# Kernel optimization log

Hardware: AMD Instinct MI355X
Metric: run time of the kernel (lower is better)

## Reference

```python
import jax, jax.numpy as jnp
import numpy as np

SEQ_LEN, BATCH, INPUT_SIZE, HIDDEN = 512, 64, 256, 1024


def setup_inputs() -> dict:
    key = jax.random.key(0)
    ks = jax.random.split(key, 17)
    inp = {"x": jax.random.normal(ks[0], (SEQ_LEN, BATCH, INPUT_SIZE), dtype=jnp.float32)}
    # 8 Linear layers: odd-numbered take x (in=INPUT_SIZE), even-numbered take h (in=HIDDEN).
    sx = 1.0 / np.sqrt(INPUT_SIZE)
    sh = 1.0 / np.sqrt(HIDDEN)
    for i in range(1, 9):
        fan_in, scale = (INPUT_SIZE, sx) if i % 2 == 1 else (HIDDEN, sh)
        inp[f"W{i}"] = jax.random.uniform(ks[2 * i - 1], (fan_in, HIDDEN), jnp.float32, -scale, scale)
        inp[f"b{i}"] = jax.random.uniform(ks[2 * i], (HIDDEN,), jnp.float32, -scale, scale)
    return inp


def reference(x, W1, b1, W2, b2, W3, b3, W4, b4, W5, b5, W6, b6, W7, b7, W8, b8):
    # Gate order matching the torch module: out1(f-like)=lin1/lin2, out2(i)=lin3/lin4,
    # out3(o)=lin5/lin6, cand=lin7/lin8.  Fuse the 4 input-side GEMMs into one big GEMM
    # over all timesteps, and the 4 hidden-side GEMMs into one per-step GEMM.
    Wx = jnp.concatenate([W1, W3, W5, W7], axis=1)            # (I, 4H)
    bx = jnp.concatenate([b1, b3, b5, b7], axis=0)            # (4H,)
    Wh = jnp.concatenate([W2, W4, W6, W8], axis=1)            # (H, 4H)
    bh = jnp.concatenate([b2, b4, b6, b8], axis=0)            # (4H,)

    H = W2.shape[0]
    xg = jnp.einsum('sbi,ig->sbg', x, Wx) + bx + bh           # (S, B, 4H)

    def step(carry, xg_t):
        h, c = carry                                          # (B, H) each
        g = xg_t + h @ Wh                                     # (B, 4H)
        f = jax.nn.sigmoid(g[:, 0 * H:1 * H])
        i = jax.nn.sigmoid(g[:, 1 * H:2 * H])
        o = jax.nn.sigmoid(g[:, 2 * H:3 * H])
        cand = jnp.tanh(g[:, 3 * H:4 * H])
        c = f * c + i * cand
        h = o * jnp.tanh(c)
        return (h, c), h

    B = x.shape[1]
    h0 = jnp.zeros((B, H), dtype=x.dtype)
    c0 = jnp.zeros((B, H), dtype=x.dtype)
    (h, c), h_seq = jax.lax.scan(step, (h0, c0), xg)
    # Torch module returns (h_seq, (h, c)) with h,c leading dim 1.
    return h_seq, (h[None], c[None])
```

## Files before the change

### kernel.cpp

```cpp
#include <hip/hip_runtime.h>


#define OFF_XB    0ul
#define OFF_WXP   16777216ul
#define OFF_WHP   18874368ul
#define OFF_BIAS  27262976ul
#define OFF_HBUF  27279360ul
#define OFF_FLG   27541504ul

typedef __attribute__((ext_vector_type(8))) __bf16 bf16x8;
typedef __attribute__((ext_vector_type(4))) float  floatx4;

struct KPtrs { const float* p[17]; };

__device__ __forceinline__ unsigned short f2bf(float f) {
  unsigned int u = __float_as_uint(f);
  u += 0x7fffu + ((u >> 16) & 1u);
  return (unsigned short)(u >> 16);
}

__device__ __forceinline__ bf16x8 ld16(const unsigned short* p) {
  return *(const bf16x8*)p;
}

__device__ __forceinline__ bf16x8 ldsys16(const unsigned short* p) {
  unsigned long long a =
      __hip_atomic_load((const unsigned long long*)p,       __ATOMIC_RELAXED, __HIP_MEMORY_SCOPE_AGENT);
  unsigned long long b =
      __hip_atomic_load((const unsigned long long*)(p + 4), __ATOMIC_RELAXED, __HIP_MEMORY_SCOPE_AGENT);
  unsigned long long arr[2] = {a, b};
  bf16x8 r;
  __builtin_memcpy(&r, arr, 16);
  return r;
}

__device__ __forceinline__ float fsig(float x) {
  return __builtin_amdgcn_rcpf(1.f + __expf(-x));
}
__device__ __forceinline__ float ftanh(float x) {
  return 1.f - 2.f * __builtin_amdgcn_rcpf(1.f + __expf(2.f * x));
}

__global__ void pack_kernel(KPtrs P, unsigned char* ws) {
  unsigned short* xb   = (unsigned short*)(ws + OFF_XB);
  unsigned short* wxp  = (unsigned short*)(ws + OFF_WXP);
  unsigned short* whp  = (unsigned short*)(ws + OFF_WHP);
  float*          bias = (float*)(ws + OFF_BIAS);
  unsigned int*   hb32 = (unsigned int*)(ws + OFF_HBUF);
  int*            flg  = (int*)(ws + OFF_FLG);
  const float* x = P.p[0];

  const long tid = (long)blockIdx.x * blockDim.x + threadIdx.x;
  const long nth = (long)gridDim.x * blockDim.x;

  for (long e = tid; e < 8388608l; e += nth)
    xb[e] = f2bf(x[e]);
  for (long e = tid; e < 1048576l; e += nth) {
    int c = (int)(e >> 8), i = (int)(e & 255);
    int gg = c >> 10, j = c & 1023;
    wxp[e] = f2bf(P.p[1 + 4 * gg][i * 1024 + j]);
  }
  for (long e = tid; e < 4194304l; e += nth) {
    int c = (int)(e >> 10), k = (int)(e & 1023);
    int gg = c >> 10, j = c & 1023;
    whp[e] = f2bf(P.p[3 + 4 * gg][k * 1024 + j]);
  }
  for (long e = tid; e < 4096l; e += nth) {
    int gg = (int)(e >> 10), j = (int)(e & 1023);
    bias[e] = P.p[2 + 4 * gg][j] + P.p[4 + 4 * gg][j];
  }
  for (long e = tid; e < 65536l; e += nth)
    __hip_atomic_store(&hb32[e], 0u, __ATOMIC_RELAXED, __HIP_MEMORY_SCOPE_AGENT);
  for (long e = tid; e < 128l; e += nth)
    __hip_atomic_store(&flg[e], -1, __ATOMIC_RELAXED, __HIP_MEMORY_SCOPE_AGENT);
}

__global__ void __launch_bounds__(256, 1)
lstm_kernel(const unsigned char* __restrict__ ws, float* __restrict__ out) {
  const unsigned short* xb   = (const unsigned short*)(ws + OFF_XB);
  const unsigned short* wxp  = (const unsigned short*)(ws + OFF_WXP);
  const unsigned short* whp  = (const unsigned short*)(ws + OFF_WHP);
  const float*          bias = (const float*)(ws + OFF_BIAS);
  unsigned short*       hbuf = (unsigned short*)(ws + OFF_HBUF);
  int*                  flg  = (int*)(ws + OFF_FLG);

  const int tid = threadIdx.x;
  const int wv = tid >> 6, lane = tid & 63;
  const int r = lane & 15, q = lane >> 4;
  const int s = blockIdx.x & 63, g = blockIdx.x >> 6;

  __shared__ float pc[4][8][64][4];

  bf16x8 whf[4][8];
  bf16x8 wxf[4][2];
#pragma unroll
  for (int nt = 0; nt < 4; ++nt) {
    const int c = nt * 1024 + s * 16 + r;
    const unsigned short* whb = whp + (long)c * 1024 + q * 8;
    const unsigned short* wxb = wxp + (long)c * 256 + q * 8;
#pragma unroll
    for (int kk = 0; kk < 8; ++kk) whf[nt][kk] = ld16(whb + wv * 256 + kk * 32);
#pragma unroll
    for (int kk = 0; kk < 2; ++kk) wxf[nt][kk] = ld16(wxb + wv * 64 + kk * 32);
  }

  const unsigned short* xa0 = xb + ((long)g * 32 + r) * 256 + q * 8;

  const int ej = tid & 15, ebp = tid >> 4;
  const int lidx = ej | ((ebp >> 2) << 4), rg = ebp & 3;
  float bs[4];
#pragma unroll
  for (int gt = 0; gt < 4; ++gt) bs[gt] = bias[gt * 1024 + s * 16 + ej];

  const unsigned long long* fl64 = (const unsigned long long*)flg;
  float cst[2] = {0.f, 0.f};

  for (int t = 0; t < 512; ++t) {
    floatx4 acc[2][4];
#pragma unroll
    for (int mt = 0; mt < 2; ++mt)
#pragma unroll
      for (int nt = 0; nt < 4; ++nt) acc[mt][nt] = (floatx4){0.f, 0.f, 0.f, 0.f};

    const unsigned short* xaT = xa0 + (long)t * (64 * 256);
#pragma unroll
    for (int kk = 0; kk < 2; ++kk) {
      const int k0 = wv * 64 + kk * 32;
      bf16x8 a0 = ld16(xaT + k0);
      bf16x8 a1 = ld16(xaT + 16 * 256 + k0);
#pragma unroll
      for (int nt = 0; nt < 4; ++nt) {
        acc[0][nt] = __builtin_amdgcn_mfma_f32_16x16x32_bf16(a0, wxf[nt][kk], acc[0][nt], 0, 0, 0);
        acc[1][nt] = __builtin_amdgcn_mfma_f32_16x16x32_bf16(a1, wxf[nt][kk], acc[1][nt], 0, 0, 0);
      }
    }

    {
      const int need = t - 1;
      while (true) {
        unsigned long long fv =
            __hip_atomic_load(&fl64[lane], __ATOMIC_RELAXED, __HIP_MEMORY_SCOPE_AGENT);
        bool ok = ((int)(unsigned int)fv >= need) && ((int)(unsigned int)(fv >> 32) >= need);
        if (__all(ok)) break;
        __builtin_amdgcn_s_sleep(1);
      }
    }
    asm volatile("" ::: "memory");

    const unsigned short* ha =
        hbuf + (long)((t - 1) & 1) * 65536 + ((long)g * 32 + r) * 1024 + q * 8;
#pragma unroll
    for (int kk = 0; kk < 8; ++kk) {
      const int k0 = wv * 256 + kk * 32;
      bf16x8 a0 = ldsys16(ha + k0);
      bf16x8 a1 = ldsys16(ha + 16 * 1024 + k0);
#pragma unroll
      for (int nt = 0; nt < 4; ++nt) {
        acc[0][nt] = __builtin_amdgcn_mfma_f32_16x16x32_bf16(a0, whf[nt][kk], acc[0][nt], 0, 0, 0);
        acc[1][nt] = __builtin_amdgcn_mfma_f32_16x16x32_bf16(a1, whf[nt][kk], acc[1][nt], 0, 0, 0);
      }
    }

#pragma unroll
    for (int mt = 0; mt < 2; ++mt)
#pragma unroll
      for (int nt = 0; nt < 4; ++nt)
        *(floatx4*)(&pc[wv][mt * 4 + nt][lane][0]) = acc[mt][nt];
    __syncthreads();

    float hv[2], cv[2];
#pragma unroll
    for (int e = 0; e < 2; ++e) {
      float gs[4];
#pragma unroll
      for (int gt = 0; gt < 4; ++gt) {
        float sv = bs[gt];
#pragma unroll
        for (int w2 = 0; w2 < 4; ++w2) sv += pc[w2][e * 4 + gt][lidx][rg];
        gs[gt] = sv;
      }
      const float f = fsig(gs[0]), ii = fsig(gs[1]), o = fsig(gs[2]);
      const float cd = ftanh(gs[3]);
      cst[e] = f * cst[e] + ii * cd;
      cv[e] = cst[e];
      hv[e] = o * ftanh(cst[e]);
    }

    int emit = ((ej & 1) == 0);
#pragma unroll
    for (int e = 0; e < 2; ++e) {
      unsigned short hb = f2bf(hv[e]);
      unsigned short nb = (unsigned short)__shfl_xor((int)hb, 1, 64);
      if (emit) {
        unsigned int pv = (unsigned int)hb | ((unsigned int)nb << 16);
        unsigned int* hp = (unsigned int*)(hbuf + (long)(t & 1) * 65536 +
                                           (g * 32 + e * 16 + ebp) * 1024 + s * 16 + ej);
        __hip_atomic_store(hp, pv, __ATOMIC_RELAXED, __HIP_MEMORY_SCOPE_AGENT);
      }
    }
    __syncthreads();
    if (tid == 0)
      __hip_atomic_store(&flg[blockIdx.x], t, __ATOMIC_RELAXED, __HIP_MEMORY_SCOPE_AGENT);

#pragma unroll
    for (int e = 0; e < 2; ++e) {
      const int bl = e * 16 + ebp;
      const long oidx = (long)t * 65536 + (g * 32 + bl) * 1024 + s * 16 + ej;
      out[oidx] = hv[e];
      if (t == 511) {
        out[33554432l + (g * 32 + bl) * 1024 + s * 16 + ej] = hv[e];
        out[33619968l + (g * 32 + bl) * 1024 + s * 16 + ej] = cv[e];
      }
    }
  }
}

extern "C" void kernel_launch(void* const* d_in, const int* in_sizes, int n_in,
                              void* d_out, int out_size, void* d_ws, size_t ws_size,
                              hipStream_t stream) {
  (void)in_sizes; (void)n_in; (void)out_size; (void)ws_size;
  KPtrs P;
  for (int i = 0; i < 17; ++i) P.p[i] = (const float*)d_in[i];
  pack_kernel<<<dim3(2048), dim3(256), 0, stream>>>(P, (unsigned char*)d_ws);
  lstm_kernel<<<dim3(128), dim3(256), 0, stream>>>((const unsigned char*)d_ws, (float*)d_out);
}
```

Before: 3.059 ms.

## Replace per-block step flags with per-element tagged hidden-state words

```diff
diff --git a/kernel.cpp b/kernel.cpp
--- a/kernel.cpp
+++ b/kernel.cpp
@@ -6,7 +6,6 @@
 #define OFF_WHP   18874368ul
 #define OFF_BIAS  27262976ul
 #define OFF_HBUF  27279360ul
-#define OFF_FLG   27541504ul
 
 typedef __attribute__((ext_vector_type(8))) __bf16 bf16x8;
 typedef __attribute__((ext_vector_type(4))) float  floatx4;
@@ -23,22 +22,48 @@
   return *(const bf16x8*)p;
 }
 
-__device__ __forceinline__ bf16x8 ldsys16(const unsigned short* p) {
-  unsigned long long a =
-      __hip_atomic_load((const unsigned long long*)p,       __ATOMIC_RELAXED, __HIP_MEMORY_SCOPE_AGENT);
-  unsigned long long b =
-      __hip_atomic_load((const unsigned long long*)(p + 4), __ATOMIC_RELAXED, __HIP_MEMORY_SCOPE_AGENT);
-  unsigned long long arr[2] = {a, b};
-  bf16x8 r;
-  __builtin_memcpy(&r, arr, 16);
-  return r;
-}
-
 __device__ __forceinline__ float fsig(float x) {
   return __builtin_amdgcn_rcpf(1.f + __expf(-x));
 }
 __device__ __forceinline__ float ftanh(float x) {
   return 1.f - 2.f * __builtin_amdgcn_rcpf(1.f + __expf(2.f * x));
+}
+
+__device__ __forceinline__ unsigned long long lduc64(const unsigned int* p) {
+  return __hip_atomic_load((const unsigned long long*)p,
+                           __ATOMIC_RELAXED, __HIP_MEMORY_SCOPE_AGENT);
+}
+
+struct Chunk8 { unsigned long long v[8]; };
+
+__device__ __forceinline__ Chunk8 ldchunk(const unsigned int* b0, const unsigned int* b1) {
+  Chunk8 c;
+#pragma unroll
+  for (int i = 0; i < 4; ++i) c.v[i]     = lduc64(b0 + 2 * i);
+#pragma unroll
+  for (int i = 0; i < 4; ++i) c.v[4 + i] = lduc64(b1 + 2 * i);
+  return c;
+}
+
+__device__ __forceinline__ bool tags_ok(const Chunk8& c, unsigned long long tt) {
+  const unsigned long long M = 0x0000FFFF0000FFFFull;
+  unsigned long long d = 0;
+#pragma unroll
+  for (int i = 0; i < 8; ++i) d |= (c.v[i] ^ tt) & M;
+  return d == 0;
+}
+
+__device__ __forceinline__ bf16x8 unpack4(const unsigned long long* v) {
+  unsigned int w[4];
+#pragma unroll
+  for (int i = 0; i < 4; ++i) {
+    unsigned int lo = (unsigned int)v[i];
+    unsigned int hi = (unsigned int)(v[i] >> 32);
+    w[i] = __builtin_amdgcn_perm(hi, lo, 0x07060302);
+  }
+  bf16x8 r;
+  __builtin_memcpy(&r, w, 16);
+  return r;
 }
 
 __global__ void pack_kernel(KPtrs P, unsigned char* ws) {
@@ -47,7 +72,6 @@
   unsigned short* whp  = (unsigned short*)(ws + OFF_WHP);
   float*          bias = (float*)(ws + OFF_BIAS);
   unsigned int*   hb32 = (unsigned int*)(ws + OFF_HBUF);
-  int*            flg  = (int*)(ws + OFF_FLG);
   const float* x = P.p[0];
 
   const long tid = (long)blockIdx.x * blockDim.x + threadIdx.x;
@@ -69,10 +93,8 @@
     int gg = (int)(e >> 10), j = (int)(e & 1023);
     bias[e] = P.p[2 + 4 * gg][j] + P.p[4 + 4 * gg][j];
   }
-  for (long e = tid; e < 65536l; e += nth)
+  for (long e = tid; e < 131072l; e += nth)
     __hip_atomic_store(&hb32[e], 0u, __ATOMIC_RELAXED, __HIP_MEMORY_SCOPE_AGENT);
-  for (long e = tid; e < 128l; e += nth)
-    __hip_atomic_store(&flg[e], -1, __ATOMIC_RELAXED, __HIP_MEMORY_SCOPE_AGENT);
 }
 
 __global__ void __launch_bounds__(256, 1)
@@ -81,15 +103,14 @@
   const unsigned short* wxp  = (const unsigned short*)(ws + OFF_WXP);
   const unsigned short* whp  = (const unsigned short*)(ws + OFF_WHP);
   const float*          bias = (const float*)(ws + OFF_BIAS);
-  unsigned short*       hbuf = (unsigned short*)(ws + OFF_HBUF);
-  int*                  flg  = (int*)(ws + OFF_FLG);
+  unsigned int*         hbuf = (unsigned int*)(ws + OFF_HBUF);
 
   const int tid = threadIdx.x;
   const int wv = tid >> 6, lane = tid & 63;
   const int r = lane & 15, q = lane >> 4;
   const int s = blockIdx.x & 63, g = blockIdx.x >> 6;
 
-  __shared__ float pc[4][8][64][4];
+  __shared__ float pc[2][4][8][64][4];
 
   bf16x8 whf[4][8];
   bf16x8 wxf[4][2];
@@ -112,15 +133,21 @@
 #pragma unroll
   for (int gt = 0; gt < 4; ++gt) bs[gt] = bias[gt * 1024 + s * 16 + ej];
 
-  const unsigned long long* fl64 = (const unsigned long long*)flg;
   float cst[2] = {0.f, 0.f};
 
   for (int t = 0; t < 512; ++t) {
+    const int pb = t & 1;
     floatx4 acc[2][4];
 #pragma unroll
     for (int mt = 0; mt < 2; ++mt)
 #pragma unroll
       for (int nt = 0; nt < 4; ++nt) acc[mt][nt] = (floatx4){0.f, 0.f, 0.f, 0.f};
+
+    const unsigned int* ha =
+        hbuf + (long)((t - 1) & 1) * 65536 + ((long)g * 32 + r) * 1024 + q * 8;
+    const int kbase = wv * 256;
+
+    Chunk8 cur = ldchunk(ha + kbase, ha + 16 * 1024 + kbase);
 
     const unsigned short* xaT = xa0 + (long)t * (64 * 256);
 #pragma unroll
@@ -135,37 +162,30 @@
       }
     }
 
-    {
-      const int need = t - 1;
-      while (true) {
-        unsigned long long fv =
-            __hip_atomic_load(&fl64[lane], __ATOMIC_RELAXED, __HIP_MEMORY_SCOPE_AGENT);
-        bool ok = ((int)(unsigned int)fv >= need) && ((int)(unsigned int)(fv >> 32) >= need);
-        if (__all(ok)) break;
-        __builtin_amdgcn_s_sleep(1);
-      }
-    }
-    asm volatile("" ::: "memory");
-
-    const unsigned short* ha =
-        hbuf + (long)((t - 1) & 1) * 65536 + ((long)g * 32 + r) * 1024 + q * 8;
+    const unsigned long long tg = (unsigned int)t;
+    const unsigned long long tt = tg | (tg << 32);
 #pragma unroll
     for (int kk = 0; kk < 8; ++kk) {
-      const int k0 = wv * 256 + kk * 32;
-      bf16x8 a0 = ldsys16(ha + k0);
-      bf16x8 a1 = ldsys16(ha + 16 * 1024 + k0);
+      const int k0 = kbase + kk * 32;
+      Chunk8 nxt;
+      if (kk < 7) nxt = ldchunk(ha + k0 + 32, ha + 16 * 1024 + k0 + 32);
+      while (!tags_ok(cur, tt))
+        cur = ldchunk(ha + k0, ha + 16 * 1024 + k0);
+      bf16x8 a0 = unpack4(&cur.v[0]);
+      bf16x8 a1 = unpack4(&cur.v[4]);
 #pragma unroll
       for (int nt = 0; nt < 4; ++nt) {
         acc[0][nt] = __builtin_amdgcn_mfma_f32_16x16x32_bf16(a0, whf[nt][kk], acc[0][nt], 0, 0, 0);
         acc[1][nt] = __builtin_amdgcn_mfma_f32_16x16x32_bf16(a1, whf[nt][kk], acc[1][nt], 0, 0, 0);
       }
+      if (kk < 7) cur = nxt;
     }
 
 #pragma unroll
     for (int mt = 0; mt < 2; ++mt)
 #pragma unroll
       for (int nt = 0; nt < 4; ++nt)
-        *(floatx4*)(&pc[wv][mt * 4 + nt][lane][0]) = acc[mt][nt];
+        *(floatx4*)(&pc[pb][wv][mt * 4 + nt][lane][0]) = acc[mt][nt];
     __syncthreads();
 
     float hv[2], cv[2];
@@ -176,7 +196,7 @@
       for (int gt = 0; gt < 4; ++gt) {
         float sv = bs[gt];
 #pragma unroll
-        for (int w2 = 0; w2 < 4; ++w2) sv += pc[w2][e * 4 + gt][lidx][rg];
+        for (int w2 = 0; w2 < 4; ++w2) sv += pc[pb][w2][e * 4 + gt][lidx][rg];
         gs[gt] = sv;
       }
       const float f = fsig(gs[0]), ii = fsig(gs[1]), o = fsig(gs[2]);
@@ -186,21 +206,21 @@
       hv[e] = o * ftanh(cst[e]);
     }
 
-    int emit = ((ej & 1) == 0);
+    const unsigned int tagw = (unsigned int)(t + 1);
+    const int emit = ((ej & 1) == 0);
 #pragma unroll
     for (int e = 0; e < 2; ++e) {
-      unsigned short hb = f2bf(hv[e]);
-      unsigned short nb = (unsigned short)__shfl_xor((int)hb, 1, 64);
+      unsigned short hb16 = f2bf(hv[e]);
+      unsigned short nb = (unsigned short)__shfl_xor((int)hb16, 1, 64);
       if (emit) {
-        unsigned int pv = (unsigned int)hb | ((unsigned int)nb << 16);
-        unsigned int* hp = (unsigned int*)(hbuf + (long)(t & 1) * 65536 +
-                                           (g * 32 + e * 16 + ebp) * 1024 + s * 16 + ej);
+        unsigned long long pv =
+            (unsigned long long)((((unsigned int)hb16) << 16) | tagw) |
+            ((unsigned long long)((((unsigned int)nb) << 16) | tagw) << 32);
+        unsigned long long* hp = (unsigned long long*)(hbuf + (long)pb * 65536 +
+            (long)(g * 32 + e * 16 + ebp) * 1024 + s * 16 + ej);
         __hip_atomic_store(hp, pv, __ATOMIC_RELAXED, __HIP_MEMORY_SCOPE_AGENT);
       }
     }
-    __syncthreads();
-    if (tid == 0)
-      __hip_atomic_store(&flg[blockIdx.x], t, __ATOMIC_RELAXED, __HIP_MEMORY_SCOPE_AGENT);
 
 #pragma unroll
     for (int e = 0; e < 2; ++e) {
```

New measurement: 5.154 ms. 68.5% more time.

## Stage recurrent weights in XOR-swizzled LDS and narrow the flag polling

Applied to the files above, without the earlier changes.

```diff
diff --git a/kernel.cpp b/kernel.cpp
--- a/kernel.cpp
+++ b/kernel.cpp
@@ -63,7 +63,8 @@
   for (long e = tid; e < 4194304l; e += nth) {
     int c = (int)(e >> 10), k = (int)(e & 1023);
     int gg = c >> 10, j = c & 1023;
-    whp[e] = f2bf(P.p[3 + 4 * gg][k * 1024 + j]);
+    long dst = ((long)c << 10) | (long)(k ^ ((c & 7) << 3));
+    whp[dst] = f2bf(P.p[3 + 4 * gg][k * 1024 + j]);
   }
   for (long e = tid; e < 4096l; e += nth) {
     int gg = (int)(e >> 10), j = (int)(e & 1023);
@@ -89,129 +90,138 @@
   const int r = lane & 15, q = lane >> 4;
   const int s = blockIdx.x & 63, g = blockIdx.x >> 6;
 
-  __shared__ float pc[4][8][64][4];
-
-  bf16x8 whf[4][8];
+  __shared__ unsigned short whl[65536];
+  __shared__ float pc[4][4][64][4];
+
+  for (int ch = tid; ch < 8192; ch += 256) {
+    const int le = ch * 8;
+    const int rl = le >> 10, k8 = le & 1023;
+    const int cg = (rl >> 4) * 1024 + s * 16 + (rl & 15);
+    *(bf16x8*)&whl[le] = ld16(whp + (long)cg * 1024 + k8);
+  }
+
   bf16x8 wxf[4][2];
 #pragma unroll
   for (int nt = 0; nt < 4; ++nt) {
     const int c = nt * 1024 + s * 16 + r;
-    const unsigned short* whb = whp + (long)c * 1024 + q * 8;
-    const unsigned short* wxb = wxp + (long)c * 256 + q * 8;
-#pragma unroll
-    for (int kk = 0; kk < 8; ++kk) whf[nt][kk] = ld16(whb + wv * 256 + kk * 32);
-#pragma unroll
-    for (int kk = 0; kk < 2; ++kk) wxf[nt][kk] = ld16(wxb + wv * 64 + kk * 32);
-  }
-
-  const unsigned short* xa0 = xb + ((long)g * 32 + r) * 256 + q * 8;
-
-  const int ej = tid & 15, ebp = tid >> 4;
-  const int lidx = ej | ((ebp >> 2) << 4), rg = ebp & 3;
+#pragma unroll
+    for (int kk = 0; kk < 2; ++kk)
+      wxf[nt][kk] = ld16(wxp + (long)c * 256 + wv * 64 + kk * 32 + q * 8);
+  }
+
+  const int ej = tid & 15, eb = tid >> 4;
+  const int lidx = ej | ((eb >> 2) << 4), rg = eb & 3;
   float bs[4];
 #pragma unroll
   for (int gt = 0; gt < 4; ++gt) bs[gt] = bias[gt * 1024 + s * 16 + ej];
 
+  const unsigned short* xa0 = xb + (long)(g * 32 + r) * 256 + q * 8;
+  const int rs = (r & 7) << 3;
   const unsigned long long* fl64 = (const unsigned long long*)flg;
+  const int fidx = g * 32 + (lane & 31);
+
   float cst[2] = {0.f, 0.f};
+  __syncthreads();
 
   for (int t = 0; t < 512; ++t) {
+    unsigned long long fv =
+        __hip_atomic_load(&fl64[fidx], __ATOMIC_RELAXED, __HIP_MEMORY_SCOPE_AGENT);
+
+    const unsigned short* xaT = xa0 + (long)t * 16384;
+    bf16x8 xv[2][2];
+#pragma unroll
+    for (int kk = 0; kk < 2; ++kk) {
+      xv[0][kk] = ld16(xaT + wv * 64 + kk * 32);
+      xv[1][kk] = ld16(xaT + 16 * 256 + wv * 64 + kk * 32);
+    }
+
     floatx4 acc[2][4];
 #pragma unroll
     for (int mt = 0; mt < 2; ++mt)
 #pragma unroll
       for (int nt = 0; nt < 4; ++nt) acc[mt][nt] = (floatx4){0.f, 0.f, 0.f, 0.f};
 
-    const unsigned short* xaT = xa0 + (long)t * (64 * 256);
-#pragma unroll
-    for (int kk = 0; kk < 2; ++kk) {
-      const int k0 = wv * 64 + kk * 32;
-      bf16x8 a0 = ld16(xaT + k0);
-      bf16x8 a1 = ld16(xaT + 16 * 256 + k0);
+#pragma unroll
+    for (int kk = 0; kk < 2; ++kk)
 #pragma unroll
       for (int nt = 0; nt < 4; ++nt) {
-        acc[0][nt] = __builtin_amdgcn_mfma_f32_16x16x32_bf16(a0, wxf[nt][kk], acc[0][nt], 0, 0, 0);
-        acc[1][nt] = __builtin_amdgcn_mfma_f32_16x16x32_bf16(a1, wxf[nt][kk], acc[1][nt], 0, 0, 0);
-      }
-    }
+        acc[0][nt] = __builtin_amdgcn_mfma_f32_16x16x32_bf16(xv[0][kk], wxf[nt][kk], acc[0][nt], 0, 0, 0);
+        acc[1][nt] = __builtin_amdgcn_mfma_f32_16x16x32_bf16(xv[1][kk], wxf[nt][kk], acc[1][nt], 0, 0, 0);
+      }
 
     {
       const int need = t - 1;
-      while (true) {
-        unsigned long long fv =
-            __hip_atomic_load(&fl64[lane], __ATOMIC_RELAXED, __HIP_MEMORY_SCOPE_AGENT);
-        bool ok = ((int)(unsigned int)fv >= need) && ((int)(unsigned int)(fv >> 32) >= need);
-        if (__all(ok)) break;
+      while (!(((int)(unsigned int)fv >= need) && ((int)(unsigned int)(fv >> 32) >= need) ?
+               __all(1) : __all(0))) {
         __builtin_amdgcn_s_sleep(1);
+        fv = __hip_atomic_load(&fl64[fidx], __ATOMIC_RELAXED, __HIP_MEMORY_SCOPE_AGENT);
       }
     }
     asm volatile("" ::: "memory");
 
     const unsigned short* ha =
         hbuf + (long)((t - 1) & 1) * 65536 + ((long)g * 32 + r) * 1024 + q * 8;
+    bf16x8 hv0[8], hv1[8];
 #pragma unroll
     for (int kk = 0; kk < 8; ++kk) {
       const int k0 = wv * 256 + kk * 32;
-      bf16x8 a0 = ldsys16(ha + k0);
-      bf16x8 a1 = ldsys16(ha + 16 * 1024 + k0);
+      hv0[kk] = ldsys16(ha + k0);
+      hv1[kk] = ldsys16(ha + 16 * 1024 + k0);
+    }
+
+#pragma unroll
+    for (int kk = 0; kk < 8; ++kk) {
+      bf16x8 wb[4];
+      const int el = wv * 256 + ((kk * 32 + q * 8) ^ rs);
+#pragma unroll
+      for (int nt = 0; nt < 4; ++nt)
+        wb[nt] = *(const bf16x8*)&whl[(nt * 16 + r) * 1024 + el];
 #pragma unroll
       for (int nt = 0; nt < 4; ++nt) {
-        acc[0][nt] = __builtin_amdgcn_mfma_f32_16x16x32_bf16(a0, whf[nt][kk], acc[0][nt], 0, 0, 0);
-        acc[1][nt] = __builtin_amdgcn_mfma_f32_16x16x32_bf16(a1, whf[nt][kk], acc[1][nt], 0, 0, 0);
-      }
-    }
-
-#pragma unroll
-    for (int mt = 0; mt < 2; ++mt)
+        acc[0][nt] = __builtin_amdgcn_mfma_f32_16x16x32_bf16(hv0[kk], wb[nt], acc[0][nt], 0, 0, 0);
+        acc[1][nt] = __builtin_amdgcn_mfma_f32_16x16x32_bf16(hv1[kk], wb[nt], acc[1][nt], 0, 0, 0);
+      }
+    }
+
+    float hvv[2];
+#pragma unroll
+    for (int e = 0; e < 2; ++e) {
+      __syncthreads();
 #pragma unroll
       for (int nt = 0; nt < 4; ++nt)
-        *(floatx4*)(&pc[wv][mt * 4 + nt][lane][0]) = acc[mt][nt];
-    __syncthreads();
-
-    float hv[2], cv[2];
-#pragma unroll
-    for (int e = 0; e < 2; ++e) {
+        *(floatx4*)(&pc[wv][nt][lane][0]) = acc[e][nt];
+      __syncthreads();
+
       float gs[4];
 #pragma unroll
-      for (int gt = 0; gt < 4; ++gt) {
-        float sv = bs[gt];
-#pragma unroll
-        for (int w2 = 0; w2 < 4; ++w2) sv += pc[w2][e * 4 + gt][lidx][rg];
-        gs[gt] = sv;
-      }
+      for (int gt = 0; gt < 4; ++gt)
+        gs[gt] = bs[gt] + pc[0][gt][lidx][rg] + pc[1][gt][lidx][rg] +
+                 pc[2][gt][lidx][rg] + pc[3][gt][lidx][rg];
       const float f = fsig(gs[0]), ii = fsig(gs[1]), o = fsig(gs[2]);
       const float cd = ftanh(gs[3]);
       cst[e] = f * cst[e] + ii * cd;
-      cv[e] = cst[e];
-      hv[e] = o * ftanh(cst[e]);
-    }
-
-    int emit = ((ej & 1) == 0);
-#pragma unroll
-    for (int e = 0; e < 2; ++e) {
-      unsigned short hb = f2bf(hv[e]);
-      unsigned short nb = (unsigned short)__shfl_xor((int)hb, 1, 64);
-      if (emit) {
-        unsigned int pv = (unsigned int)hb | ((unsigned int)nb << 16);
+      hvv[e] = o * ftanh(cst[e]);
+
+      unsigned short hb16 = f2bf(hvv[e]);
+      unsigned short nbv = (unsigned short)__shfl_xor((int)hb16, 1, 64);
+      if ((ej & 1) == 0) {
+        unsigned int pv = (unsigned int)hb16 | ((unsigned int)nbv << 16);
         unsigned int* hp = (unsigned int*)(hbuf + (long)(t & 1) * 65536 +
-                                           (g * 32 + e * 16 + ebp) * 1024 + s * 16 + ej);
+            (long)(g * 32 + e * 16 + eb) * 1024 + s * 16 + ej);
         __hip_atomic_store(hp, pv, __ATOMIC_RELAXED, __HIP_MEMORY_SCOPE_AGENT);
       }
-    }
+
+      const long ob = (long)(g * 32 + e * 16 + eb) * 1024 + s * 16 + ej;
+      out[(long)t * 65536 + ob] = hvv[e];
+      if (t == 511) {
+        out[33554432l + ob] = hvv[e];
+        out[33619968l + ob] = cst[e];
+      }
+    }
+
     __syncthreads();
     if (tid == 0)
       __hip_atomic_store(&flg[blockIdx.x], t, __ATOMIC_RELAXED, __HIP_MEMORY_SCOPE_AGENT);
-
-#pragma unroll
-    for (int e = 0; e < 2; ++e) {
-      const int bl = e * 16 + ebp;
-      const long oidx = (long)t * 65536 + (g * 32 + bl) * 1024 + s * 16 + ej;
-      out[oidx] = hv[e];
-      if (t == 511) {
-        out[33554432l + (g * 32 + bl) * 1024 + s * 16 + ej] = hv[e];
-        out[33619968l + (g * 32 + bl) * 1024 + s * 16 + ej] = cv[e];
-      }
-    }
   }
 }
 
```

After: 3.702 ms. 21.0% more time.
